# Kernel tuning notes

Hardware: AMD Instinct MI355X
Metric: run time of the kernel (lower is better)

The kernel has to match this reference:

```python
import jax, jax.numpy as jnp
import numpy as np

HIDDEN = 1024
B, S = 4, 2048

def setup_inputs() -> dict:
    key = jax.random.key(0)
    k1, k2 = jax.random.split(key)
    qkv = jax.random.normal(k1, (B, S, HIDDEN), dtype=jnp.float32)
    mask = jnp.ones((B, S), dtype=jnp.float32)
    W_qkv = jax.random.normal(k2, (HIDDEN, 3 * HIDDEN), dtype=jnp.float32) * (HIDDEN ** -0.5)
    b_qkv = jnp.zeros((3 * HIDDEN,), dtype=jnp.float32)
    return {"qkv": qkv, "mask": mask, "W_qkv": W_qkv, "b_qkv": b_qkv}

def reference(qkv, mask, W_qkv, b_qkv):
    scale = HIDDEN ** -0.5
    proj = jnp.einsum("bsi,ih->bsh", qkv, W_qkv) + b_qkv  # [B,S,3H]
    q, k, v = jnp.split(proj, 3, axis=-1)                  # each [B,S,H]
    q = q * scale
    scores = jnp.einsum("bqh,bkh->bqk", q, k)              # [B,S,S]
    scores = scores + (1.0 - mask)[:, None, :] * -10000.0
    dist = jax.nn.softmax(scores, axis=-1)                 # dropout = identity (eval)
    return jnp.einsum("bqk,bkh->bqh", dist, v)             # [B,S,H]
```

## Files before the change

### kernel.cpp

```cpp
#include <hip/hip_runtime.h>
#include <hip/hip_bf16.h>

#define HID   1024
#define H3    3072
#define SEQ   2048
#define NB    4
#define MTOT  8192

typedef __bf16 bf16;
typedef bf16  bf16x4 __attribute__((ext_vector_type(4)));
typedef bf16  bf16x8 __attribute__((ext_vector_type(8)));
typedef float f32x4  __attribute__((ext_vector_type(4)));

#define MFMA16(a, b, c) __builtin_amdgcn_mfma_f32_16x16x32_bf16((a), (b), (c), 0, 0, 0)

#define GLOAD_LDS16(gp, lp)                                                     \
    __builtin_amdgcn_global_load_lds(                                           \
        (const __attribute__((address_space(1))) void*)(gp),                    \
        (__attribute__((address_space(3))) void*)(lp), 16, 0, 0)

#define FENCE() asm volatile("" ::: "memory")

__device__ __forceinline__ void stage_half(
    const bf16* __restrict__ G, long ld, long row0, long col0,
    char* dstbase, int w, int lane)
{
    const int r  = lane >> 2;
    const int c0 = ((lane & 3) * 8) ^ (((lane >> 5) & 1) << 4);
#pragma unroll
    for (int l = 0; l < 2; ++l) {
        const int sh = l * 8 + w;
        const bf16* src = G + (row0 + (long)((sh >> 1) * 16 + r)) * ld
                            + col0 + ((sh & 1) * 32 + c0);
        GLOAD_LDS16(src, dstbase + sh * 1024);
    }
}

__device__ __forceinline__ void gemm256_core(
    const bf16* __restrict__ A, long lda,
    const bf16* __restrict__ Bt, long ldb,
    long m0, long n0, int NT, char* lds, f32x4 (&acc)[8][4])
{
    const int tid = threadIdx.x, lane = tid & 63, w = tid >> 6;
    const int lr = lane & 15, lkg = lane >> 4;
    const int subA = (w >> 2) * 8;
    const int subB = (w & 3) * 4;
    const int inner = lr * 64 + (((lkg * 8) ^ ((lr >> 3) << 4)) << 1);

    char* A0b = lds;
    char* B0b = lds + 32768;
    char* A1b = lds + 65536;
    char* B1b = lds + 98304;

    stage_half(A,  lda, m0,        0, A0b,          w, lane);
    stage_half(A,  lda, m0 + 128,  0, A0b + 16384,  w, lane);
    stage_half(Bt, ldb, n0,        0, B0b,          w, lane);
    stage_half(Bt, ldb, n0 + 128,  0, B0b + 16384,  w, lane);
    stage_half(Bt, ldb, n0,       64, B1b,          w, lane);
    stage_half(Bt, ldb, n0 + 128, 64, B1b + 16384,  w, lane);
    asm volatile("s_waitcnt vmcnt(0)" ::: "memory");
    __builtin_amdgcn_s_barrier();
    FENCE();

    bf16x8 aR[4][2], bR[4][2];

    for (int t = 0; t < NT; ++t) {
        char* Ac = (t & 1) ? A1b : A0b;
        char* Bc = (t & 1) ? B1b : B0b;
        char* An = (t & 1) ? A0b : A1b;
        const long kA = (long)(t + 1) * 64;
        const long kB = (long)(t + 2) * 64;
        const bool doA = (t + 1 < NT), doB = (t + 2 < NT);

#pragma unroll
        for (int mf = 0; mf < 4; ++mf)
#pragma unroll
            for (int ks = 0; ks < 2; ++ks)
                aR[mf][ks] = *(const bf16x8*)(Ac + ((subA + mf) * 2 + ks) * 1024 + inner);
#pragma unroll
        for (int nf = 0; nf < 2; ++nf)
#pragma unroll
            for (int ks = 0; ks < 2; ++ks)
                bR[nf][ks] = *(const bf16x8*)(Bc + ((subB + nf) * 2 + ks) * 1024 + inner);
        if (doA) stage_half(A, lda, m0, kA, An, w, lane);
        __builtin_amdgcn_s_barrier();
        __builtin_amdgcn_s_setprio(1);
#pragma unroll
        for (int mf = 0; mf < 4; ++mf)
#pragma unroll
            for (int nf = 0; nf < 2; ++nf)
#pragma unroll
                for (int ks = 0; ks < 2; ++ks)
                    acc[mf][nf] = MFMA16(aR[mf][ks], bR[nf][ks], acc[mf][nf]);
        __builtin_amdgcn_s_setprio(0);
        __builtin_amdgcn_s_barrier();
        FENCE();

#pragma unroll
        for (int nf = 0; nf < 2; ++nf)
#pragma unroll
            for (int ks = 0; ks < 2; ++ks)
                bR[2 + nf][ks] = *(const bf16x8*)(Bc + ((subB + 2 + nf) * 2 + ks) * 1024 + inner);
        if (doA) stage_half(A, lda, m0 + 128, kA, An + 16384, w, lane);
        __builtin_amdgcn_s_barrier();
        __builtin_amdgcn_s_setprio(1);
#pragma unroll
        for (int mf = 0; mf < 4; ++mf)
#pragma unroll
            for (int nf = 0; nf < 2; ++nf)
#pragma unroll
                for (int ks = 0; ks < 2; ++ks)
                    acc[mf][2 + nf] = MFMA16(aR[mf][ks], bR[2 + nf][ks], acc[mf][2 + nf]);
        __builtin_amdgcn_s_setprio(0);
        __builtin_amdgcn_s_barrier();
        FENCE();

#pragma unroll
        for (int mf = 0; mf < 4; ++mf)
#pragma unroll
            for (int ks = 0; ks < 2; ++ks)
                aR[mf][ks] = *(const bf16x8*)(Ac + ((subA + 4 + mf) * 2 + ks) * 1024 + inner);
        if (doB) stage_half(Bt, ldb, n0, kB, Bc, w, lane);
        __builtin_amdgcn_s_barrier();
        __builtin_amdgcn_s_setprio(1);
#pragma unroll
        for (int mf = 0; mf < 4; ++mf)
#pragma unroll
            for (int nf = 0; nf < 2; ++nf)
#pragma unroll
                for (int ks = 0; ks < 2; ++ks)
                    acc[4 + mf][nf] = MFMA16(aR[mf][ks], bR[nf][ks], acc[4 + mf][nf]);
        __builtin_amdgcn_s_setprio(0);
        __builtin_amdgcn_s_barrier();
        FENCE();

        if (doB) {
            stage_half(Bt, ldb, n0 + 128, kB, Bc + 16384, w, lane);
            asm volatile("s_waitcnt vmcnt(4)" ::: "memory");
        } else {
            asm volatile("s_waitcnt vmcnt(0)" ::: "memory");
        }
        __builtin_amdgcn_s_barrier();
        __builtin_amdgcn_s_setprio(1);
#pragma unroll
        for (int mf = 0; mf < 4; ++mf)
#pragma unroll
            for (int nf = 0; nf < 2; ++nf)
#pragma unroll
                for (int ks = 0; ks < 2; ++ks)
                    acc[4 + mf][2 + nf] = MFMA16(aR[mf][ks], bR[2 + nf][ks], acc[4 + mf][2 + nf]);
        __builtin_amdgcn_s_setprio(0);
        __builtin_amdgcn_s_barrier();
        FENCE();
    }
}

__device__ __forceinline__ void gemm_h_core(
    const bf16* __restrict__ A, long lda,
    const bf16* __restrict__ Bt, long ldb,
    long m0, long n0, int NT, char* lds, f32x4 (&acc)[4][4])
{
    const int tid = threadIdx.x, lane = tid & 63, w = tid >> 6;
    const int lr = lane & 15, lkg = lane >> 4;
    const int subA = (w >> 2) * 4;
    const int subB = (w & 3) * 4;
    const int inner = lr * 64 + (((lkg * 8) ^ ((lr >> 3) << 4)) << 1);

    char* A0b = lds;
    char* B0b = lds + 16384;
    char* A1b = lds + 49152;
    char* B1b = lds + 65536;

    stage_half(A,  lda, m0,        0, A0b,          w, lane);
    stage_half(Bt, ldb, n0,        0, B0b,          w, lane);
    stage_half(Bt, ldb, n0 + 128,  0, B0b + 16384,  w, lane);
    stage_half(Bt, ldb, n0,       64, B1b,          w, lane);
    stage_half(Bt, ldb, n0 + 128, 64, B1b + 16384,  w, lane);
    asm volatile("s_waitcnt vmcnt(0)" ::: "memory");
    __builtin_amdgcn_s_barrier();
    FENCE();

    bf16x8 aR[2][2], bR[4][2];

    for (int t = 0; t < NT; ++t) {
        char* Ac = (t & 1) ? A1b : A0b;
        char* Bc = (t & 1) ? B1b : B0b;
        char* An = (t & 1) ? A0b : A1b;
        const long kA = (long)(t + 1) * 64;
        const long kB = (long)(t + 2) * 64;
        const bool doA = (t + 1 < NT), doB = (t + 2 < NT);

#pragma unroll
        for (int mf = 0; mf < 2; ++mf)
#pragma unroll
            for (int ks = 0; ks < 2; ++ks)
                aR[mf][ks] = *(const bf16x8*)(Ac + ((subA + mf) * 2 + ks) * 1024 + inner);
#pragma unroll
        for (int nf = 0; nf < 2; ++nf)
#pragma unroll
            for (int ks = 0; ks < 2; ++ks)
                bR[nf][ks] = *(const bf16x8*)(Bc + ((subB + nf) * 2 + ks) * 1024 + inner);
        if (doA) stage_half(A, lda, m0, kA, An, w, lane);
        __builtin_amdgcn_s_barrier();
        __builtin_amdgcn_s_setprio(1);
#pragma unroll
        for (int mf = 0; mf < 2; ++mf)
#pragma unroll
            for (int nf = 0; nf < 2; ++nf)
#pragma unroll
                for (int ks = 0; ks < 2; ++ks)
                    acc[mf][nf] = MFMA16(aR[mf][ks], bR[nf][ks], acc[mf][nf]);
        __builtin_amdgcn_s_setprio(0);
        __builtin_amdgcn_s_barrier();
        FENCE();

#pragma unroll
        for (int nf = 0; nf < 2; ++nf)
#pragma unroll
            for (int ks = 0; ks < 2; ++ks)
                bR[2 + nf][ks] = *(const bf16x8*)(Bc + ((subB + 2 + nf) * 2 + ks) * 1024 + inner);
        __builtin_amdgcn_s_barrier();
        __builtin_amdgcn_s_setprio(1);
#pragma unroll
        for (int mf = 0; mf < 2; ++mf)
#pragma unroll
            for (int nf = 0; nf < 2; ++nf)
#pragma unroll
                for (int ks = 0; ks < 2; ++ks)
                    acc[mf][2 + nf] = MFMA16(aR[mf][ks], bR[2 + nf][ks], acc[mf][2 + nf]);
        __builtin_amdgcn_s_setprio(0);
        __builtin_amdgcn_s_barrier();
        FENCE();

#pragma unroll
        for (int mf = 0; mf < 2; ++mf)
#pragma unroll
            for (int ks = 0; ks < 2; ++ks)
                aR[mf][ks] = *(const bf16x8*)(Ac + ((subA + 2 + mf) * 2 + ks) * 1024 + inner);
        if (doB) {
            stage_half(Bt, ldb, n0,       kB, Bc,         w, lane);
            stage_half(Bt, ldb, n0 + 128, kB, Bc + 16384, w, lane);
        }
        __builtin_amdgcn_s_barrier();
        __builtin_amdgcn_s_setprio(1);
#pragma unroll
        for (int mf = 0; mf < 2; ++mf)
#pragma unroll
            for (int nf = 0; nf < 2; ++nf)
#pragma unroll
                for (int ks = 0; ks < 2; ++ks)
                    acc[2 + mf][nf] = MFMA16(aR[mf][ks], bR[nf][ks], acc[2 + mf][nf]);
        __builtin_amdgcn_s_setprio(0);
        __builtin_amdgcn_s_barrier();
        FENCE();

        if (doB) {
            asm volatile("s_waitcnt vmcnt(4)" ::: "memory");
        } else {
            asm volatile("s_waitcnt vmcnt(0)" ::: "memory");
        }
        __builtin_amdgcn_s_barrier();
        __builtin_amdgcn_s_setprio(1);
#pragma unroll
        for (int mf = 0; mf < 2; ++mf)
#pragma unroll
            for (int nf = 0; nf < 2; ++nf)
#pragma unroll
                for (int ks = 0; ks < 2; ++ks)
                    acc[2 + mf][2 + nf] = MFMA16(aR[mf][ks], bR[2 + nf][ks], acc[2 + mf][2 + nf]);
        __builtin_amdgcn_s_setprio(0);
        __builtin_amdgcn_s_barrier();
        FENCE();
    }
}

__global__ __launch_bounds__(256) void conv_kernel(
    const float* __restrict__ X, const float* __restrict__ W,
    bf16* __restrict__ Xb, bf16* __restrict__ Wt, float* __restrict__ lbuf)
{
    __shared__ bf16 T[64][66];
    const int bid = blockIdx.x;
    if (bid < 4096) {
        const long i = ((long)bid * 256 + threadIdx.x) * 8;
        float4 a = *(const float4*)(X + i);
        float4 b = *(const float4*)(X + i + 4);
        bf16x8 o;
        o[0] = (bf16)a.x; o[1] = (bf16)a.y; o[2] = (bf16)a.z; o[3] = (bf16)a.w;
        o[4] = (bf16)b.x; o[5] = (bf16)b.y; o[6] = (bf16)b.z; o[7] = (bf16)b.w;
        *(bf16x8*)(Xb + i) = o;
    } else if (bid < 4096 + 768) {
        const int b2 = bid - 4096;
        const int n0 = (b2 % 48) * 64, k0 = (b2 / 48) * 64;
        const int r = threadIdx.x >> 2, s = threadIdx.x & 3;
        const float* wp = W + (size_t)(k0 + r) * H3 + n0 + s * 16;
#pragma unroll
        for (int q = 0; q < 4; ++q) {
            float4 a = *(const float4*)(wp + q * 4);
            T[r][s * 16 + q * 4 + 0] = (bf16)a.x;
            T[r][s * 16 + q * 4 + 1] = (bf16)a.y;
            T[r][s * 16 + q * 4 + 2] = (bf16)a.z;
            T[r][s * 16 + q * 4 + 3] = (bf16)a.w;
        }
        __syncthreads();
        bf16x8 o0, o1;
#pragma unroll
        for (int i = 0; i < 8; ++i) o0[i] = T[s * 16 + i][r];
#pragma unroll
        for (int i = 0; i < 8; ++i) o1[i] = T[s * 16 + 8 + i][r];
        bf16* op = Wt + (size_t)(n0 + r) * HID + k0 + s * 16;
        *(bf16x8*)op       = o0;
        *(bf16x8*)(op + 8) = o1;
    } else {
        for (int i = threadIdx.x; i < MTOT; i += 256) lbuf[i] = 0.0f;
    }
}

__global__ __launch_bounds__(512, 2) void proj_mixed(
    const bf16* __restrict__ Xb, const bf16* __restrict__ Wt,
    const float* __restrict__ bias,
    bf16* __restrict__ Qb, bf16* __restrict__ Kb, bf16* __restrict__ Vt)
{
    __shared__ __attribute__((aligned(16))) char lds[135168];
    const int bid = blockIdx.x;
    const int tid = threadIdx.x, lane = tid & 63, w = tid >> 6;
    const int lr = lane & 15, lkg = lane >> 4;

    if (bid < 256) {
        const int x = bid & 7, q = bid >> 3;
        const int bm = x * 4 + (q & 3);
        const int bn = q >> 2;
        f32x4 acc[8][4] = {};
        gemm256_core(Xb, HID, Wt, HID, (long)bm * 256, (long)bn * 256, 16, lds, acc);

        const int wmL = (w >> 2) * 128;
        const int wnL = (w & 3) * 64;
        const int seg = bn >> 2;

        __syncthreads();
        bf16* sm_ = (bf16*)lds;
        const float qs = (seg == 0) ? 0.03125f : 1.0f;
#pragma unroll
        for (int nf = 0; nf < 4; ++nf) {
            const int nl = wnL + nf * 16 + lr;
            const float bv = bias[bn * 256 + nl];
#pragma unroll
            for (int mf = 0; mf < 8; ++mf) {
                const int ml = wmL + mf * 16 + lkg * 4;
#pragma unroll
                for (int j = 0; j < 4; ++j)
                    sm_[(ml + j) * 264 + nl] = (bf16)((acc[mf][nf][j] + bv) * qs);
            }
        }
        __syncthreads();
        bf16* dst = (seg == 0) ? Qb : Kb;
        const long rowbase = (long)bm * 256;
        const long colbase = (long)(bn & 3) * 256;
#pragma unroll
        for (int it = 0; it < 16; ++it) {
            const int ml = (tid >> 5) + it * 16;
            const int nc = (tid & 31) * 8;
            bf16x8 vv = *(const bf16x8*)&sm_[ml * 264 + nc];
            *(bf16x8*)&dst[(rowbase + ml) * HID + colbase + nc] = vv;
        }
    } else {
        const int b2 = bid - 256;
        const int x = b2 & 7, q2 = b2 >> 3;
        const int vm = x * 8 + (q2 & 7);
        const int vn = q2 >> 3;
        f32x4 acc[4][4] = {};
        gemm_h_core(Xb, HID, Wt, HID, (long)vm * 128, 2048 + (long)vn * 256,
                    16, lds, acc);

        const int wmL = (w >> 2) * 64;
        const int wnL = (w & 3) * 64;

        __syncthreads();
        bf16* sm_ = (bf16*)lds;
#pragma unroll
        for (int nf = 0; nf < 4; ++nf) {
            const int nl = wnL + nf * 16 + lr;
            const float bv = bias[2048 + vn * 256 + nl];
#pragma unroll
            for (int mf = 0; mf < 4; ++mf) {
                const int ml = wmL + mf * 16 + lkg * 4;
                bf16x4 pk;
#pragma unroll
                for (int j = 0; j < 4; ++j) pk[j] = (bf16)(acc[mf][nf][j] + bv);
                *(bf16x4*)&sm_[nl * 136 + ml] = pk;
            }
        }
        __syncthreads();
        const int  bb = vm >> 4;
        const long s0 = (long)(vm & 15) * 128;
        const long h0 = (long)vn * 256;
#pragma unroll
        for (int it = 0; it < 8; ++it) {
            const int nl = (tid >> 4) + it * 32;
            const int mc = (tid & 15) * 8;
            bf16x8 vv = *(const bf16x8*)&sm_[nl * 136 + mc];
            *(bf16x8*)&Vt[((long)(bb << 10) + h0 + nl) * SEQ + s0 + mc] = vv;
        }
    }
}

__global__ __launch_bounds__(512, 2) void qk_gemm2(
    const bf16* __restrict__ Qb, const bf16* __restrict__ Kb,
    bf16* __restrict__ Pb, float* __restrict__ lbuf,
    const float* __restrict__ mask, int b_base)
{
    __shared__ __attribute__((aligned(16))) char lds[135168];
    __shared__ float lsum[2][128][4];
    const int z = blockIdx.z, b = b_base + z;

    f32x4 acc[8][4] = {};
    gemm256_core(Qb + (size_t)b * SEQ * HID, HID,
                 Kb + (size_t)b * SEQ * HID, HID,
                 (long)blockIdx.x * 256, (long)blockIdx.y * 256, 16, lds, acc);

    const int tid = threadIdx.x, lane = tid & 63, w = tid >> 6;
    const int lr = lane & 15, lkg = lane >> 4;
    const int mh = w >> 2;
    const int nw = w & 3;

    __syncthreads();
    bf16* smP = (bf16*)lds;

    float mterm[4];
#pragma unroll
    for (int nf = 0; nf < 4; ++nf) {
        const int col = (int)blockIdx.y * 256 + nw * 64 + nf * 16 + lr;
        mterm[nf] = (1.0f - mask[(size_t)b * SEQ + col]) * -10000.0f;
    }

#pragma unroll
    for (int mf = 0; mf < 8; ++mf) {
#pragma unroll
        for (int j = 0; j < 4; ++j) {
            const int rloc = mf * 16 + lkg * 4 + j;
            float rs = 0.0f;
#pragma unroll
            for (int nf = 0; nf < 4; ++nf) {
                const float e = __expf(acc[mf][nf][j] + mterm[nf]);
                smP[(mh * 128 + rloc) * 264 + nw * 64 + nf * 16 + lr] = (bf16)e;
                rs += e;
            }
            rs += __shfl_xor(rs, 1);
            rs += __shfl_xor(rs, 2);
            rs += __shfl_xor(rs, 4);
            rs += __shfl_xor(rs, 8);
            if (lr == 0) lsum[mh][rloc][nw] = rs;
        }
    }
    __syncthreads();

    bf16* P = Pb + (size_t)z * SEQ * SEQ;
    const long rowbase = (long)blockIdx.x * 256;
    const long colbase = (long)blockIdx.y * 256;
#pragma unroll
    for (int it = 0; it < 16; ++it) {
        const int ml = (tid >> 5) + it * 16;
        const int nc = (tid & 31) * 8;
        bf16x8 vv = *(const bf16x8*)&smP[ml * 264 + nc];
        *(bf16x8*)&P[(rowbase + ml) * SEQ + colbase + nc] = vv;
    }

    if (tid < 256) {
        const int half = tid >> 7, r128 = tid & 127;
        const float s4 = lsum[half][r128][0] + lsum[half][r128][1]
                       + lsum[half][r128][2] + lsum[half][r128][3];
        atomicAdd(&lbuf[(size_t)b * SEQ + rowbase + tid], s4);
    }
}

__global__ __launch_bounds__(512, 2) void pv_gemm2(
    const bf16* __restrict__ Pb, const bf16* __restrict__ Vt,
    const float* __restrict__ lbuf, float* __restrict__ out, int b_base)
{
    __shared__ __attribute__((aligned(16))) char lds[98304];
    const int z = blockIdx.z, b = b_base + z;

    f32x4 acc[4][4] = {};
    gemm_h_core(Pb + (size_t)z * SEQ * SEQ, SEQ,
                Vt + (size_t)b * HID * SEQ, SEQ,
                (long)blockIdx.x * 128, (long)blockIdx.y * 256, 32, lds, acc);

    const int tid = threadIdx.x, lane = tid & 63, w = tid >> 6;
    const int lr = lane & 15, lkg = lane >> 4;
    const int m0i = (int)blockIdx.x * 128 + (w >> 2) * 64;
    const int n0i = (int)blockIdx.y * 256 + (w & 3) * 64;
    float* C = out + (size_t)b * SEQ * HID;
#pragma unroll
    for (int mf = 0; mf < 4; ++mf)
#pragma unroll
        for (int j = 0; j < 4; ++j) {
            const int row = m0i + mf * 16 + lkg * 4 + j;
            const float inv = 1.0f / lbuf[(size_t)b * SEQ + row];
#pragma unroll
            for (int nf = 0; nf < 4; ++nf)
                C[(size_t)row * HID + n0i + nf * 16 + lr] = acc[mf][nf][j] * inv;
        }
}

extern "C" void kernel_launch(void* const* d_in, const int* in_sizes, int n_in,
                              void* d_out, int out_size, void* d_ws, size_t ws_size,
                              hipStream_t stream)
{
    const float* X    = (const float*)d_in[0];
    const float* mask = (const float*)d_in[1];
    const float* W    = (const float*)d_in[2];
    const float* bias = (const float*)d_in[3];
    float* out = (float*)d_out;

    char* ws = (char*)d_ws;
    const size_t MB = 1024 * 1024;
    bf16*  Qb   = (bf16*)ws;
    bf16*  Kb   = (bf16*)(ws + 16 * MB);
    bf16*  Vt   = (bf16*)(ws + 32 * MB);
    float* lbuf = (float*)(ws + 48 * MB);
    bf16*  Xb   = (bf16*)(ws + 49 * MB);
    bf16*  Wt   = (bf16*)(ws + 65 * MB);
    bf16*  Pb   = (bf16*)(ws + 49 * MB);

    int nbg;
    if      (ws_size >= 81 * MB) nbg = 4;
    else if (ws_size >= 65 * MB) nbg = 2;
    else                         nbg = 1;

    conv_kernel<<<4096 + 768 + 1, 256, 0, stream>>>(X, W, Xb, Wt, lbuf);
    proj_mixed<<<512, 512, 0, stream>>>(Xb, Wt, bias, Qb, Kb, Vt);

    for (int g = 0; g < NB / nbg; ++g) {
        const int b0 = g * nbg;
        qk_gemm2<<<dim3(8, 8, nbg), 512, 0, stream>>>(Qb, Kb, Pb, lbuf, mask, b0);
        pv_gemm2<<<dim3(16, 4, nbg), 512, 0, stream>>>(Pb, Vt, lbuf, out, b0);
    }
}
```

Before: 153.1 us.

## Load B operand directly from global into registers, bypassing LDS in 256-tile GEMM

Replaces the shared 256x256 GEMM core with a variant that stages only the A tile through LDS and has each wave read its B fragments straight from global memory into double-buffered registers, prefetched one k-step ahead. The goal is to halve LDS traffic and LDS footprint and to remove the B staging barriers. Block-index mapping for the projection and QK kernels also changes to a flat grid with column-fastest ordering. In exchange it raises register pressure and relies on uncoalesced-ish 16-byte global loads per lane, with B tiles now re-read by every wave group instead of shared.

```diff
diff --git a/kernel.cpp b/kernel.cpp
--- a/kernel.cpp
+++ b/kernel.cpp
@@ -36,7 +36,74 @@
     }
 }
 
-__device__ __forceinline__ void gemm256_core(
+#define QK_TILE(t, Ac, An, CLo, CHi, NLo, NHi)                                 \
+{                                                                              \
+    const bool doP = ((t) + 1 < NT);                                           \
+    const long kA = (long)((t) + 1) * 64;                                      \
+    const long bo = (long)((t) + 1) * 64;                                      \
+                        \
+    _Pragma("unroll") for (int mf = 0; mf < 4; ++mf)                           \
+    _Pragma("unroll") for (int ks = 0; ks < 2; ++ks)                           \
+        aR[mf][ks] = *(const bf16x8*)((Ac) + ((subA + mf) * 2 + ks) * 1024 + inner); \
+    if (doP) stage_half(A, lda, m0, kA, (An), w, lane);                        \
+    __builtin_amdgcn_s_barrier();                                              \
+    __builtin_amdgcn_s_setprio(1);                                             \
+    _Pragma("unroll") for (int mf = 0; mf < 4; ++mf)                           \
+    _Pragma("unroll") for (int nf = 0; nf < 2; ++nf)                           \
+    _Pragma("unroll") for (int ks = 0; ks < 2; ++ks)                           \
+        acc[mf][nf] = MFMA16(aR[mf][ks], CLo[nf][ks], acc[mf][nf]);            \
+    __builtin_amdgcn_s_setprio(0);                                             \
+    __builtin_amdgcn_s_barrier();                                              \
+    FENCE();                                                                   \
+                            \
+    if (doP) {                                                                 \
+        _Pragma("unroll") for (int nf = 0; nf < 2; ++nf)                       \
+        _Pragma("unroll") for (int ks = 0; ks < 2; ++ks)                       \
+            NLo[nf][ks] = *(const bf16x8*)(bp + bo + nf * nstep + ks * 32);    \
+    }                                                                          \
+    __builtin_amdgcn_s_barrier();                                              \
+    __builtin_amdgcn_s_setprio(1);                                             \
+    _Pragma("unroll") for (int mf = 0; mf < 4; ++mf)                           \
+    _Pragma("unroll") for (int nf = 0; nf < 2; ++nf)                           \
+    _Pragma("unroll") for (int ks = 0; ks < 2; ++ks)                           \
+        acc[mf][2 + nf] = MFMA16(aR[mf][ks], CHi[nf][ks], acc[mf][2 + nf]);    \
+    __builtin_amdgcn_s_setprio(0);                                             \
+    __builtin_amdgcn_s_barrier();                                              \
+    FENCE();                                                                   \
+                        \
+    _Pragma("unroll") for (int mf = 0; mf < 4; ++mf)                           \
+    _Pragma("unroll") for (int ks = 0; ks < 2; ++ks)                           \
+        aR[mf][ks] = *(const bf16x8*)((Ac) + ((subA + 4 + mf) * 2 + ks) * 1024 + inner); \
+    if (doP) stage_half(A, lda, m0 + 128, kA, (An) + 16384, w, lane);          \
+    __builtin_amdgcn_s_barrier();                                              \
+    __builtin_amdgcn_s_setprio(1);                                             \
+    _Pragma("unroll") for (int mf = 0; mf < 4; ++mf)                           \
+    _Pragma("unroll") for (int nf = 0; nf < 2; ++nf)                           \
+    _Pragma("unroll") for (int ks = 0; ks < 2; ++ks)                           \
+        acc[4 + mf][nf] = MFMA16(aR[mf][ks], CLo[nf][ks], acc[4 + mf][nf]);    \
+    __builtin_amdgcn_s_setprio(0);                                             \
+    __builtin_amdgcn_s_barrier();                                              \
+    FENCE();                                                                   \
+             \
+    if (doP) {                                                                 \
+        _Pragma("unroll") for (int nf = 0; nf < 2; ++nf)                       \
+        _Pragma("unroll") for (int ks = 0; ks < 2; ++ks)                       \
+            NHi[nf][ks] = *(const bf16x8*)(bp + bo + (2 + nf) * nstep + ks * 32); \
+    }                                                                          \
+    __builtin_amdgcn_s_barrier();                                              \
+    __builtin_amdgcn_s_setprio(1);                                             \
+    _Pragma("unroll") for (int mf = 0; mf < 4; ++mf)                           \
+    _Pragma("unroll") for (int nf = 0; nf < 2; ++nf)                           \
+    _Pragma("unroll") for (int ks = 0; ks < 2; ++ks)                           \
+        acc[4 + mf][2 + nf] = MFMA16(aR[mf][ks], CHi[nf][ks], acc[4 + mf][2 + nf]); \
+    __builtin_amdgcn_s_setprio(0);                                             \
+    if (doP) { asm volatile("s_waitcnt vmcnt(4)" ::: "memory"); }              \
+    else     { asm volatile("s_waitcnt vmcnt(0)" ::: "memory"); }              \
+    __builtin_amdgcn_s_barrier();                                              \
+    FENCE();                                                                   \
+}
+
+__device__ __forceinline__ void gemm256_bd(
     const bf16* __restrict__ A, long lda,
     const bf16* __restrict__ Bt, long ldb,
     long m0, long n0, int NT, char* lds, f32x4 (&acc)[8][4])
@@ -44,114 +111,32 @@
     const int tid = threadIdx.x, lane = tid & 63, w = tid >> 6;
     const int lr = lane & 15, lkg = lane >> 4;
     const int subA = (w >> 2) * 8;
-    const int subB = (w & 3) * 4;
     const int inner = lr * 64 + (((lkg * 8) ^ ((lr >> 3) << 4)) << 1);
 
     char* A0b = lds;
-    char* B0b = lds + 32768;
-    char* A1b = lds + 65536;
-    char* B1b = lds + 98304;
-
-    stage_half(A,  lda, m0,        0, A0b,          w, lane);
-    stage_half(A,  lda, m0 + 128,  0, A0b + 16384,  w, lane);
-    stage_half(Bt, ldb, n0,        0, B0b,          w, lane);
-    stage_half(Bt, ldb, n0 + 128,  0, B0b + 16384,  w, lane);
-    stage_half(Bt, ldb, n0,       64, B1b,          w, lane);
-    stage_half(Bt, ldb, n0 + 128, 64, B1b + 16384,  w, lane);
+    char* A1b = lds + 32768;
+
+    const bf16* bp = Bt + (n0 + (long)(w & 3) * 64 + lr) * ldb + lkg * 8;
+    const long nstep = 16 * ldb;
+
+    stage_half(A, lda, m0,       0, A0b,         w, lane);
+    stage_half(A, lda, m0 + 128, 0, A0b + 16384, w, lane);
+    bf16x8 bS0[2][2], bS1[2][2], bS2[2][2], bS3[2][2];
+#pragma unroll
+    for (int nf = 0; nf < 2; ++nf)
+#pragma unroll
+        for (int ks = 0; ks < 2; ++ks) {
+            bS0[nf][ks] = *(const bf16x8*)(bp + nf * nstep + ks * 32);
+            bS1[nf][ks] = *(const bf16x8*)(bp + (2 + nf) * nstep + ks * 32);
+        }
     asm volatile("s_waitcnt vmcnt(0)" ::: "memory");
     __builtin_amdgcn_s_barrier();
     FENCE();
 
-    bf16x8 aR[4][2], bR[4][2];
-
-    for (int t = 0; t < NT; ++t) {
-        char* Ac = (t & 1) ? A1b : A0b;
-        char* Bc = (t & 1) ? B1b : B0b;
-        char* An = (t & 1) ? A0b : A1b;
-        const long kA = (long)(t + 1) * 64;
-        const long kB = (long)(t + 2) * 64;
-        const bool doA = (t + 1 < NT), doB = (t + 2 < NT);
-
-#pragma unroll
-        for (int mf = 0; mf < 4; ++mf)
-#pragma unroll
-            for (int ks = 0; ks < 2; ++ks)
-                aR[mf][ks] = *(const bf16x8*)(Ac + ((subA + mf) * 2 + ks) * 1024 + inner);
-#pragma unroll
-        for (int nf = 0; nf < 2; ++nf)
-#pragma unroll
-            for (int ks = 0; ks < 2; ++ks)
-                bR[nf][ks] = *(const bf16x8*)(Bc + ((subB + nf) * 2 + ks) * 1024 + inner);
-        if (doA) stage_half(A, lda, m0, kA, An, w, lane);
-        __builtin_amdgcn_s_barrier();
-        __builtin_amdgcn_s_setprio(1);
-#pragma unroll
-        for (int mf = 0; mf < 4; ++mf)
-#pragma unroll
-            for (int nf = 0; nf < 2; ++nf)
-#pragma unroll
-                for (int ks = 0; ks < 2; ++ks)
-                    acc[mf][nf] = MFMA16(aR[mf][ks], bR[nf][ks], acc[mf][nf]);
-        __builtin_amdgcn_s_setprio(0);
-        __builtin_amdgcn_s_barrier();
-        FENCE();
-
-#pragma unroll
-        for (int nf = 0; nf < 2; ++nf)
-#pragma unroll
-            for (int ks = 0; ks < 2; ++ks)
-                bR[2 + nf][ks] = *(const bf16x8*)(Bc + ((subB + 2 + nf) * 2 + ks) * 1024 + inner);
-        if (doA) stage_half(A, lda, m0 + 128, kA, An + 16384, w, lane);
-        __builtin_amdgcn_s_barrier();
-        __builtin_amdgcn_s_setprio(1);
-#pragma unroll
-        for (int mf = 0; mf < 4; ++mf)
-#pragma unroll
-            for (int nf = 0; nf < 2; ++nf)
-#pragma unroll
-                for (int ks = 0; ks < 2; ++ks)
-                    acc[mf][2 + nf] = MFMA16(aR[mf][ks], bR[2 + nf][ks], acc[mf][2 + nf]);
-        __builtin_amdgcn_s_setprio(0);
-        __builtin_amdgcn_s_barrier();
-        FENCE();
-
-#pragma unroll
-        for (int mf = 0; mf < 4; ++mf)
-#pragma unroll
-            for (int ks = 0; ks < 2; ++ks)
-                aR[mf][ks] = *(const bf16x8*)(Ac + ((subA + 4 + mf) * 2 + ks) * 1024 + inner);
-        if (doB) stage_half(Bt, ldb, n0, kB, Bc, w, lane);
-        __builtin_amdgcn_s_barrier();
-        __builtin_amdgcn_s_setprio(1);
-#pragma unroll
-        for (int mf = 0; mf < 4; ++mf)
-#pragma unroll
-            for (int nf = 0; nf < 2; ++nf)
-#pragma unroll
-                for (int ks = 0; ks < 2; ++ks)
-                    acc[4 + mf][nf] = MFMA16(aR[mf][ks], bR[nf][ks], acc[4 + mf][nf]);
-        __builtin_amdgcn_s_setprio(0);
-        __builtin_amdgcn_s_barrier();
-        FENCE();
-
-        if (doB) {
-            stage_half(Bt, ldb, n0 + 128, kB, Bc + 16384, w, lane);
-            asm volatile("s_waitcnt vmcnt(4)" ::: "memory");
-        } else {
-            asm volatile("s_waitcnt vmcnt(0)" ::: "memory");
-        }
-        __builtin_amdgcn_s_barrier();
-        __builtin_amdgcn_s_setprio(1);
-#pragma unroll
-        for (int mf = 0; mf < 4; ++mf)
-#pragma unroll
-            for (int nf = 0; nf < 2; ++nf)
-#pragma unroll
-                for (int ks = 0; ks < 2; ++ks)
-                    acc[4 + mf][2 + nf] = MFMA16(aR[mf][ks], bR[2 + nf][ks], acc[4 + mf][2 + nf]);
-        __builtin_amdgcn_s_setprio(0);
-        __builtin_amdgcn_s_barrier();
-        FENCE();
+    bf16x8 aR[4][2];
+    for (int t = 0; t < NT; t += 2) {
+        QK_TILE(t,     A0b, A1b, bS0, bS1, bS2, bS3);
+        QK_TILE(t + 1, A1b, A0b, bS2, bS3, bS0, bS1);
     }
 }
 
@@ -326,11 +311,10 @@
     const int lr = lane & 15, lkg = lane >> 4;
 
     if (bid < 256) {
-        const int x = bid & 7, q = bid >> 3;
-        const int bm = x * 4 + (q & 3);
-        const int bn = q >> 2;
+        const int bn = bid & 7;
+        const int bm = bid >> 3;
         f32x4 acc[8][4] = {};
-        gemm256_core(Xb, HID, Wt, HID, (long)bm * 256, (long)bn * 256, 16, lds, acc);
+        gemm256_bd(Xb, HID, Wt, HID, (long)bm * 256, (long)bn * 256, 16, lds, acc);
 
         const int wmL = (w >> 2) * 128;
         const int wnL = (w & 3) * 64;
@@ -411,11 +395,13 @@
     __shared__ __attribute__((aligned(16))) char lds[135168];
     __shared__ float lsum[2][128][4];
     const int z = blockIdx.z, b = b_base + z;
+    const int bn = (int)blockIdx.x & 7;
+    const int bm = (int)blockIdx.x >> 3;
 
     f32x4 acc[8][4] = {};
-    gemm256_core(Qb + (size_t)b * SEQ * HID, HID,
-                 Kb + (size_t)b * SEQ * HID, HID,
-                 (long)blockIdx.x * 256, (long)blockIdx.y * 256, 16, lds, acc);
+    gemm256_bd(Qb + (size_t)b * SEQ * HID, HID,
+               Kb + (size_t)b * SEQ * HID, HID,
+               (long)bm * 256, (long)bn * 256, 16, lds, acc);
 
     const int tid = threadIdx.x, lane = tid & 63, w = tid >> 6;
     const int lr = lane & 15, lkg = lane >> 4;
@@ -428,7 +414,7 @@
     float mterm[4];
 #pragma unroll
     for (int nf = 0; nf < 4; ++nf) {
-        const int col = (int)blockIdx.y * 256 + nw * 64 + nf * 16 + lr;
+        const int col = bn * 256 + nw * 64 + nf * 16 + lr;
         mterm[nf] = (1.0f - mask[(size_t)b * SEQ + col]) * -10000.0f;
     }
 
@@ -454,8 +440,8 @@
     __syncthreads();
 
     bf16* P = Pb + (size_t)z * SEQ * SEQ;
-    const long rowbase = (long)blockIdx.x * 256;
-    const long colbase = (long)blockIdx.y * 256;
+    const long rowbase = (long)bm * 256;
+    const long colbase = (long)bn * 256;
 #pragma unroll
     for (int it = 0; it < 16; ++it) {
         const int ml = (tid >> 5) + it * 16;
@@ -531,7 +517,7 @@
 
     for (int g = 0; g < NB / nbg; ++g) {
         const int b0 = g * nbg;
-        qk_gemm2<<<dim3(8, 8, nbg), 512, 0, stream>>>(Qb, Kb, Pb, lbuf, mask, b0);
+        qk_gemm2<<<dim3(64, 1, nbg), 512, 0, stream>>>(Qb, Kb, Pb, lbuf, mask, b0);
         pv_gemm2<<<dim3(16, 4, nbg), 512, 0, stream>>>(Pb, Vt, lbuf, out, b0);
     }
 }
```

After: 184.2 us. 1.2x slower.
